# Kernel optimization log

Hardware: AMD Instinct MI355X
Metric: run time of the kernel (lower is better)

The kernel has to match this reference:

```python
import jax, jax.numpy as jnp
import numpy as np

N_NODES = 50000
N_EDGES = 800000
IN_F = 128
OUT_F = 64
ALPHA = 0.2  # LeakyReLU negative slope


def setup_inputs() -> dict:
    key = jax.random.key(0)
    k_h, k_e, k_w, k_b, k_a = jax.random.split(key, 5)
    h = jax.random.normal(k_h, (N_NODES, IN_F), dtype=jnp.float32)
    adj = jax.random.randint(k_e, (2, N_EDGES), 0, N_NODES, dtype=jnp.int64)
    # Linear(in_features, out_features): weight [out, in], bias [out]
    W_w = jax.random.normal(k_w, (OUT_F, IN_F), dtype=jnp.float32) * (1.0 / np.sqrt(IN_F))
    W_b = jax.random.normal(k_b, (OUT_F,), dtype=jnp.float32) * 0.01
    a = jax.random.normal(k_a, (1, 2 * OUT_F), dtype=jnp.float32) * (1.0 / np.sqrt(2 * OUT_F))
    return {"h": h, "adj": adj, "W_w": W_w, "W_b": W_b, "a": a}


def reference(h, adj, W_w, W_b, a):
    N = h.shape[0]
    F_out = W_w.shape[0]
    inv_sqrt_f = 1.0 / float(np.sqrt(F_out))

    data = h @ W_w.T + W_b                      # [N, F_out]
    src, dst = adj[0], adj[1]

    # a @ [data[src] || data[dst]]^T  == (data @ a_src)[src] + (data @ a_dst)[dst]
    a_src, a_dst = a[0, :F_out], a[0, F_out:]
    score = (data @ a_src)[src] + (data @ a_dst)[dst]       # [E]
    edge_e = jnp.exp(jax.nn.leaky_relu(score, ALPHA) * inv_sqrt_f)

    # sparse rowsum over source rows (duplicate edges sum, matching COO semantics)
    rowsum = jax.ops.segment_sum(edge_e, src, num_segments=N)  # [N]
    row_zero = rowsum == 0.0
    rowsum = jnp.where(row_zero, 1.0, rowsum)

    # sparse mm: sum_e edge_e * data[dst] into row src; zero rows get a unit self-loop
    h_prime = jax.ops.segment_sum(edge_e[:, None] * data[dst], src, num_segments=N)
    h_prime = h_prime + row_zero[:, None].astype(data.dtype) * data
    return h_prime / rowsum[:, None]
```

## Files before the change

### kernel.cpp

```cpp
#include <hip/hip_runtime.h>
#include <math.h>

#define IN_F 128
#define OUT_F 64
#define ALPHA 0.2f
#define INV_SQRT_F 0.125f
#define CAP 64
#define BINSH 7
#define BINSZ 128
#define CAPB 4096
#define HS 136

typedef _Float16 h8  __attribute__((ext_vector_type(8)));
typedef float    f4  __attribute__((ext_vector_type(4)));

__device__ __forceinline__ float edge_w(float sc) {
    float lr = sc > 0.f ? sc : ALPHA * sc;
    return __expf(lr * INV_SQRT_F);
}

__device__ __forceinline__ h8 cvt8(float4 a, float4 b) {
    h8 r;
    r[0] = (_Float16)a.x; r[1] = (_Float16)a.y;
    r[2] = (_Float16)a.z; r[3] = (_Float16)a.w;
    r[4] = (_Float16)b.x; r[5] = (_Float16)b.y;
    r[6] = (_Float16)b.z; r[7] = (_Float16)b.w;
    return r;
}

__global__ __launch_bounds__(256) void k_p1(
    const float* __restrict__ h, const float* __restrict__ W,
    const float* __restrict__ b, const float* __restrict__ a,
    const int* __restrict__ src, const int* __restrict__ dst,
    int* __restrict__ gcur, unsigned* __restrict__ pk,
    _Float16* __restrict__ data_h,
    float* __restrict__ s_src, float* __restrict__ s_dst,
    int n_nodes, int n_edges, int g_p1)
{
    __shared__ _Float16 wsh[OUT_F * HS];
    __shared__ int hist[512];
    __shared__ int off[512];
    const int tid = threadIdx.x;

    if ((int)blockIdx.x < g_p1) {
        const int nbins = (n_nodes + BINSZ - 1) >> BINSH;
        const int e0 = (int)blockIdx.x * 4096 + tid * 16;

        for (int i = tid; i < nbins; i += 256) hist[i] = 0;
        __syncthreads();

        int s[16], d[16];
        const bool full = (e0 + 16 <= n_edges);
        if (full) {
            #pragma unroll
            for (int c = 0; c < 4; ++c) {
                int4 s4 = *(const int4*)&src[e0 + c * 4];
                int4 d4 = *(const int4*)&dst[e0 + c * 4];
                s[c*4+0] = s4.x; s[c*4+1] = s4.y; s[c*4+2] = s4.z; s[c*4+3] = s4.w;
                d[c*4+0] = d4.x; d[c*4+1] = d4.y; d[c*4+2] = d4.z; d[c*4+3] = d4.w;
            }
            #pragma unroll
            for (int i = 0; i < 16; ++i)
                atomicAdd(&hist[s[i] >> BINSH], 1);
        } else {
            #pragma unroll
            for (int i = 0; i < 16; ++i) {
                int e = e0 + i;
                s[i] = (e < n_edges) ? src[e] : -1;
                d[i] = (e < n_edges) ? dst[e] : 0;
                if (s[i] >= 0) atomicAdd(&hist[s[i] >> BINSH], 1);
            }
        }
        __syncthreads();

        for (int i = tid; i < nbins; i += 256) {
            int c = hist[i];
            off[i] = (c > 0) ? atomicAdd(&gcur[i], c) : 0;
            hist[i] = 0;
        }
        __syncthreads();

        #pragma unroll
        for (int i = 0; i < 16; ++i) {
            if (s[i] < 0) continue;
            int bin = s[i] >> BINSH;
            int r = atomicAdd(&hist[bin], 1);
            int p = off[bin] + r;
            if (p < CAPB)
                pk[(size_t)bin * CAPB + p] =
                    ((unsigned)(s[i] & (BINSZ - 1)) << 16) | (unsigned)d[i];
        }
        return;
    }

    const int node0 = ((int)blockIdx.x - g_p1) * 64;

    for (int i = tid * 8; i < OUT_F * IN_F; i += 2048) {
        int f = i >> 7, k = i & 127;
        float4 va = *(const float4*)&W[i];
        float4 vb = *(const float4*)&W[i + 4];
        *(h8*)&wsh[f * HS + k] = cvt8(va, vb);
    }
    __syncthreads();

    const int wv  = tid >> 6;
    const int lane = tid & 63;
    const int q   = lane >> 4;
    const int col = lane & 15;
    const int r0  = wv * 16;

    const int arow = min(node0 + r0 + col, n_nodes - 1);
    const float* __restrict__ hrow = h + (size_t)arow * IN_F;

    f4 acc[4] = {{0.f,0.f,0.f,0.f},{0.f,0.f,0.f,0.f},
                 {0.f,0.f,0.f,0.f},{0.f,0.f,0.f,0.f}};
    #pragma unroll
    for (int kk = 0; kk < 4; ++kk) {
        const int ko = kk * 32 + q * 8;
        float4 ha = *(const float4*)&hrow[ko];
        float4 hb = *(const float4*)&hrow[ko + 4];
        h8 av = cvt8(ha, hb);
        #pragma unroll
        for (int ct = 0; ct < 4; ++ct) {
            h8 bv = *(const h8*)&wsh[(ct * 16 + col) * HS + ko];
            acc[ct] = __builtin_amdgcn_mfma_f32_16x16x32_f16(av, bv, acc[ct], 0, 0, 0);
        }
    }

    float bb[4], as_[4], ad_[4];
    #pragma unroll
    for (int ct = 0; ct < 4; ++ct) {
        bb[ct]  = b[ct * 16 + col];
        as_[ct] = a[ct * 16 + col];
        ad_[ct] = a[OUT_F + ct * 16 + col];
    }
    #pragma unroll
    for (int reg = 0; reg < 4; ++reg) {
        int n = node0 + r0 + q * 4 + reg;
        float vv[4], ps = 0.f, pd = 0.f;
        #pragma unroll
        for (int ct = 0; ct < 4; ++ct) {
            float v = acc[ct][reg] + bb[ct];
            vv[ct] = v;
            ps = fmaf(v, as_[ct], ps);
            pd = fmaf(v, ad_[ct], pd);
        }
        #pragma unroll
        for (int m = 1; m <= 8; m <<= 1) {
            ps += __shfl_xor(ps, m, 64);
            pd += __shfl_xor(pd, m, 64);
        }
        if (n < n_nodes) {
            size_t base = (size_t)n * OUT_F + col;
            #pragma unroll
            for (int ct = 0; ct < 4; ++ct)
                data_h[base + ct * 16] = (_Float16)vv[ct];
            if (col == 0) { s_src[n] = ps; s_dst[n] = pd; }
        }
    }
}

__global__ __launch_bounds__(512) void k_bin(
    const unsigned* __restrict__ pk, const int* __restrict__ gcur,
    const float* __restrict__ s_src, const float* __restrict__ s_dst,
    const _Float16* __restrict__ data_h, float* __restrict__ out, int n_nodes)
{
    __shared__ unsigned short dbl[64 * CAP];
    __shared__ int lcnt[64];
    const int bin  = (int)blockIdx.x >> 1;
    const int half = (int)blockIdx.x & 1;
    const int tid  = threadIdx.x;

    if (tid < 64) lcnt[tid] = 0;
    __syncthreads();

    const int ecnt = min(gcur[bin], CAPB);
    for (int i = tid; i < ecnt; i += 512) {
        unsigned v = pk[(size_t)bin * CAPB + i];
        int sl = (int)(v >> 16);
        if ((sl >> 6) == half) {
            int r = atomicAdd(&lcnt[sl & 63], 1);
            if (r < CAP) dbl[(sl & 63) * CAP + r] = (unsigned short)(v & 0xffffu);
        }
    }
    __syncthreads();

    const int wv = tid >> 6, lane = tid & 63;
    const int g  = lane >> 3;
    const int fl = lane & 7;

    #pragma unroll 1
    for (int ni = 0; ni < 8; ++ni) {
        const int nl = wv * 8 + ni;
        const int n = bin * BINSZ + half * 64 + nl;
        if (n >= n_nodes) break;
        const int cn = min(lcnt[nl], CAP);
        const float ssrc = s_src[n];
        const int bbase = nl * CAP;

        float ac[8] = {0.f,0.f,0.f,0.f,0.f,0.f,0.f,0.f};
        float rs = 0.f;
        int t = 0;
        for (; t + 16 <= cn; t += 16) {
            int d0 = (int)dbl[bbase + t + g];
            int d1 = (int)dbl[bbase + t + 8 + g];
            float w0 = edge_w(ssrc + s_dst[d0]);
            float w1 = edge_w(ssrc + s_dst[d1]);
            h8 x0 = *(const h8*)&data_h[(size_t)d0 * OUT_F + 8 * fl];
            h8 x1 = *(const h8*)&data_h[(size_t)d1 * OUT_F + 8 * fl];
            #pragma unroll
            for (int i = 0; i < 8; ++i) ac[i] = fmaf(w0, (float)x0[i], ac[i]);
            #pragma unroll
            for (int i = 0; i < 8; ++i) ac[i] = fmaf(w1, (float)x1[i], ac[i]);
            rs += w0 + w1;
        }
        for (; t + 8 <= cn; t += 8) {
            int d0 = (int)dbl[bbase + t + g];
            float w0 = edge_w(ssrc + s_dst[d0]);
            h8 x0 = *(const h8*)&data_h[(size_t)d0 * OUT_F + 8 * fl];
            #pragma unroll
            for (int i = 0; i < 8; ++i) ac[i] = fmaf(w0, (float)x0[i], ac[i]);
            rs += w0;
        }
        const int rem = cn - t;
        if (g < rem) {
            int d0 = (int)dbl[bbase + t + g];
            float w0 = edge_w(ssrc + s_dst[d0]);
            h8 x0 = *(const h8*)&data_h[(size_t)d0 * OUT_F + 8 * fl];
            #pragma unroll
            for (int i = 0; i < 8; ++i) ac[i] = fmaf(w0, (float)x0[i], ac[i]);
            rs += w0;
        }
        #pragma unroll
        for (int m = 8; m <= 32; m <<= 1) {
            #pragma unroll
            for (int i = 0; i < 8; ++i) ac[i] += __shfl_xor(ac[i], m, 64);
            rs += __shfl_xor(rs, m, 64);
        }

        if (g == 0) {
            size_t o = (size_t)n * OUT_F + 8 * fl;
            f4 r0, r1;
            if (rs == 0.f) {
                h8 xv = *(const h8*)&data_h[o];
                r0[0] = (float)xv[0]; r0[1] = (float)xv[1];
                r0[2] = (float)xv[2]; r0[3] = (float)xv[3];
                r1[0] = (float)xv[4]; r1[1] = (float)xv[5];
                r1[2] = (float)xv[6]; r1[3] = (float)xv[7];
            } else {
                float inv = 1.f / rs;
                r0[0] = ac[0] * inv; r0[1] = ac[1] * inv;
                r0[2] = ac[2] * inv; r0[3] = ac[3] * inv;
                r1[0] = ac[4] * inv; r1[1] = ac[5] * inv;
                r1[2] = ac[6] * inv; r1[3] = ac[7] * inv;
            }
            __builtin_nontemporal_store(r0, (f4*)&out[o]);
            __builtin_nontemporal_store(r1, (f4*)&out[o + 4]);
        }
    }
}

extern "C" void kernel_launch(void* const* d_in, const int* in_sizes, int n_in,
                              void* d_out, int out_size, void* d_ws, size_t ws_size,
                              hipStream_t stream)
{
    const float* h   = (const float*)d_in[0];
    const int*   adj = (const int*)  d_in[1];
    const float* W   = (const float*)d_in[2];
    const float* b   = (const float*)d_in[3];
    const float* a   = (const float*)d_in[4];
    float* out = (float*)d_out;

    const int n_nodes = in_sizes[0] / IN_F;
    const int n_edges = in_sizes[1] / 2;
    const int* src = adj;
    const int* dst = adj + n_edges;
    const int nbins = (n_nodes + BINSZ - 1) >> BINSH;

    char* p = (char*)d_ws;
    _Float16*       data_h = (_Float16*)p;       p += (size_t)n_nodes * OUT_F * 2;
    unsigned*       pk     = (unsigned*)p;       p += (size_t)nbins * CAPB * 4;
    float*          s_src  = (float*)p;          p += (size_t)n_nodes * 4;
    float*          s_dst  = (float*)p;          p += (size_t)n_nodes * 4;
    int*            gcur   = (int*)p;            p += (size_t)nbins * 4;

    (void)hipMemsetAsync(gcur, 0, (size_t)nbins * sizeof(int), stream);

    const int g_p1  = (n_edges + 4095) / 4096;
    const int g_lin = (n_nodes + 63) / 64;
    k_p1<<<g_p1 + g_lin, 256, 0, stream>>>(
        h, W, b, a, src, dst, gcur, pk, data_h, s_src, s_dst,
        n_nodes, n_edges, g_p1);

    k_bin<<<nbins * 2, 512, 0, stream>>>(
        pk, gcur, s_src, s_dst, data_h, out, n_nodes);
}
```

Baseline: 123.5 us.

## Replace global atomic bin offsets with per-block fixed sub-slots and counts

The binning pass no longer builds a histogram and reserves space with global atomics. Each edge block now writes its edges for a bin into a private fixed-size sub-slot of 64 entries and stores a per-(bin,block) count. The memset and one sync phase go away. The gather kernel now scans every block's sub-slot for its bin, which is 196×64 slots per bin, mostly empty, instead of the compacted list. Edges are dropped if a block holds more than 64 for one bin, and the pk buffer grows considerably.

```diff
diff --git a/kernel.cpp b/kernel.cpp
--- a/kernel.cpp
+++ b/kernel.cpp
@@ -8,7 +8,8 @@
 #define CAP 64
 #define BINSH 7
 #define BINSZ 128
-#define CAPB 4096
+#define SUBSH 6
+#define SUBCAP 64
 #define HS 136
 
 typedef _Float16 h8  __attribute__((ext_vector_type(8)));
@@ -32,19 +33,20 @@
     const float* __restrict__ h, const float* __restrict__ W,
     const float* __restrict__ b, const float* __restrict__ a,
     const int* __restrict__ src, const int* __restrict__ dst,
-    int* __restrict__ gcur, unsigned* __restrict__ pk,
+    int* __restrict__ bcnt, unsigned* __restrict__ pk,
     _Float16* __restrict__ data_h,
     float* __restrict__ s_src, float* __restrict__ s_dst,
     int n_nodes, int n_edges, int g_p1)
 {
     __shared__ _Float16 wsh[OUT_F * HS];
     __shared__ int hist[512];
-    __shared__ int off[512];
     const int tid = threadIdx.x;
 
     if ((int)blockIdx.x < g_p1) {
         const int nbins = (n_nodes + BINSZ - 1) >> BINSH;
-        const int e0 = (int)blockIdx.x * 4096 + tid * 16;
+        const int nblk  = g_p1;
+        const int blk   = (int)blockIdx.x;
+        const int e0    = blk * 4096 + tid * 16;
 
         for (int i = tid; i < nbins; i += 256) hist[i] = 0;
         __syncthreads();
@@ -59,37 +61,28 @@
                 s[c*4+0] = s4.x; s[c*4+1] = s4.y; s[c*4+2] = s4.z; s[c*4+3] = s4.w;
                 d[c*4+0] = d4.x; d[c*4+1] = d4.y; d[c*4+2] = d4.z; d[c*4+3] = d4.w;
             }
-            #pragma unroll
-            for (int i = 0; i < 16; ++i)
-                atomicAdd(&hist[s[i] >> BINSH], 1);
         } else {
             #pragma unroll
             for (int i = 0; i < 16; ++i) {
                 int e = e0 + i;
                 s[i] = (e < n_edges) ? src[e] : -1;
                 d[i] = (e < n_edges) ? dst[e] : 0;
-                if (s[i] >= 0) atomicAdd(&hist[s[i] >> BINSH], 1);
-            }
-        }
-        __syncthreads();
-
-        for (int i = tid; i < nbins; i += 256) {
-            int c = hist[i];
-            off[i] = (c > 0) ? atomicAdd(&gcur[i], c) : 0;
-            hist[i] = 0;
-        }
-        __syncthreads();
+            }
+        }
 
         #pragma unroll
         for (int i = 0; i < 16; ++i) {
             if (s[i] < 0) continue;
             int bin = s[i] >> BINSH;
             int r = atomicAdd(&hist[bin], 1);
-            int p = off[bin] + r;
-            if (p < CAPB)
-                pk[(size_t)bin * CAPB + p] =
+            if (r < SUBCAP)
+                pk[((size_t)bin * nblk + blk) << SUBSH | (unsigned)r] =
                     ((unsigned)(s[i] & (BINSZ - 1)) << 16) | (unsigned)d[i];
         }
+        __syncthreads();
+
+        for (int i = tid; i < nbins; i += 256)
+            bcnt[i * nblk + blk] = min(hist[i], SUBCAP);
         return;
     }
 
@@ -161,26 +154,33 @@
 }
 
 __global__ __launch_bounds__(512) void k_bin(
-    const unsigned* __restrict__ pk, const int* __restrict__ gcur,
+    const unsigned* __restrict__ pk, const int* __restrict__ bcnt,
     const float* __restrict__ s_src, const float* __restrict__ s_dst,
-    const _Float16* __restrict__ data_h, float* __restrict__ out, int n_nodes)
+    const _Float16* __restrict__ data_h, float* __restrict__ out,
+    int n_nodes, int nblk)
 {
     __shared__ unsigned short dbl[64 * CAP];
     __shared__ int lcnt[64];
+    __shared__ int bcl[256];
     const int bin  = (int)blockIdx.x >> 1;
     const int half = (int)blockIdx.x & 1;
     const int tid  = threadIdx.x;
 
     if (tid < 64) lcnt[tid] = 0;
+    for (int i = tid; i < nblk; i += 512) bcl[i] = bcnt[bin * nblk + i];
     __syncthreads();
 
-    const int ecnt = min(gcur[bin], CAPB);
-    for (int i = tid; i < ecnt; i += 512) {
-        unsigned v = pk[(size_t)bin * CAPB + i];
-        int sl = (int)(v >> 16);
-        if ((sl >> 6) == half) {
-            int r = atomicAdd(&lcnt[sl & 63], 1);
-            if (r < CAP) dbl[(sl & 63) * CAP + r] = (unsigned short)(v & 0xffffu);
+    const int nslots = nblk << SUBSH;
+    const size_t pbase = ((size_t)bin * nblk) << SUBSH;
+    for (int i = tid; i < nslots; i += 512) {
+        int blk = i >> SUBSH, r = i & (SUBCAP - 1);
+        if (r < bcl[blk]) {
+            unsigned v = pk[pbase + i];
+            int sl = (int)(v >> 16);
+            if ((sl >> 6) == half) {
+                int rr = atomicAdd(&lcnt[sl & 63], 1);
+                if (rr < CAP) dbl[(sl & 63) * CAP + rr] = (unsigned short)(v & 0xffffu);
+            }
         }
     }
     __syncthreads();
@@ -276,22 +276,20 @@
     const int* src = adj;
     const int* dst = adj + n_edges;
     const int nbins = (n_nodes + BINSZ - 1) >> BINSH;
+    const int g_p1  = (n_edges + 4095) / 4096;
 
     char* p = (char*)d_ws;
     _Float16*       data_h = (_Float16*)p;       p += (size_t)n_nodes * OUT_F * 2;
-    unsigned*       pk     = (unsigned*)p;       p += (size_t)nbins * CAPB * 4;
+    unsigned*       pk     = (unsigned*)p;       p += ((size_t)nbins * g_p1 << SUBSH) * 4;
+    int*            bcnt   = (int*)p;            p += (size_t)nbins * g_p1 * 4;
     float*          s_src  = (float*)p;          p += (size_t)n_nodes * 4;
     float*          s_dst  = (float*)p;          p += (size_t)n_nodes * 4;
-    int*            gcur   = (int*)p;            p += (size_t)nbins * 4;
-
-    (void)hipMemsetAsync(gcur, 0, (size_t)nbins * sizeof(int), stream);
-
-    const int g_p1  = (n_edges + 4095) / 4096;
+
     const int g_lin = (n_nodes + 63) / 64;
     k_p1<<<g_p1 + g_lin, 256, 0, stream>>>(
-        h, W, b, a, src, dst, gcur, pk, data_h, s_src, s_dst,
+        h, W, b, a, src, dst, bcnt, pk, data_h, s_src, s_dst,
         n_nodes, n_edges, g_p1);
 
     k_bin<<<nbins * 2, 512, 0, stream>>>(
-        pk, gcur, s_src, s_dst, data_h, out, n_nodes);
-}
+        pk, bcnt, s_src, s_dst, data_h, out, n_nodes, g_p1);
+}
```

Measured after the change: 127.9 us. 3.5% more time.
